# Kernel tuning notes

Hardware: AMD Instinct MI355X
Metric: run time of the kernel (lower is better)

Reference implementation:

```python
import jax, jax.numpy as jnp
import numpy as np

KH, KW = 7, 7            # extraction kernel
EH, EW = 5, 5            # effective (cropped) kernel
PAD = (KH - EH) // 2     # = 1
EPS = 1e-7


def _extract_patches(x):
    # x: [B,H,W,C] -> patches [B,Ho,Wo,KH,KW,C], stride 1, VALID padding
    B, H, Wd, C = x.shape
    Ho, Wo = H - KH + 1, Wd - KW + 1
    rows = []
    for i in range(KH):
        cols = [x[:, i:i + Ho, j:j + Wo, :] for j in range(KW)]
        rows.append(jnp.stack(cols, axis=3))          # [B,Ho,Wo,KW,C]
    return jnp.stack(rows, axis=3)                     # [B,Ho,Wo,KH,KW,C]


def _rotate_bilinear(patches, angles):
    # patches: [N,KH,KW,C]; angles: [N]. Mirrors tf.contrib.image
    # angles_to_projective_transforms + transform(BILINEAR, fill=0).
    # Note: the layer's det(matrix)==0 NEAREST fallback never fires (det==1).
    N = patches.shape[0]
    c, s = jnp.cos(angles), jnp.sin(angles)
    Wm1, Hm1 = jnp.float32(KW - 1), jnp.float32(KH - 1)
    xo = (Wm1 - (c * Wm1 - s * Hm1)) * 0.5
    yo = (Hm1 - (s * Wm1 + c * Hm1)) * 0.5
    scale = jnp.float32(1.0 + EPS)   # transforms /= transforms[:,8:9]+1e-7
    a0, a1, a2 = c / scale, -s / scale, xo / scale
    a3, a4, a5 = s / scale, c / scale, yo / scale
    yg, xg = jnp.meshgrid(jnp.arange(KH, dtype=jnp.float32),
                          jnp.arange(KW, dtype=jnp.float32), indexing='ij')
    x_in = a0[:, None, None] * xg + a1[:, None, None] * yg + a2[:, None, None]
    y_in = a3[:, None, None] * xg + a4[:, None, None] * yg + a5[:, None, None]
    x0f = jnp.floor(x_in); y0f = jnp.floor(y_in)
    wx1 = x_in - x0f; wx0 = 1.0 - wx1
    wy1 = y_in - y0f; wy0 = 1.0 - wy1
    x0 = x0f.astype(jnp.int32); x1 = x0 + 1
    y0 = y0f.astype(jnp.int32); y1 = y0 + 1
    nidx = jnp.arange(N)[:, None, None]

    def corner(yi, xi, w):
        valid = ((xi >= 0) & (xi < KW) & (yi >= 0) & (yi < KH)).astype(patches.dtype)
        v = patches[nidx, jnp.clip(yi, 0, KH - 1), jnp.clip(xi, 0, KW - 1)]
        return (w * valid)[..., None] * v

    return (corner(y0, x0, wy0 * wx0) + corner(y0, x1, wy0 * wx1) +
            corner(y1, x0, wy1 * wx0) + corner(y1, x1, wy1 * wx1))


def reference(x, W, b):
    B, H, Wd, C = x.shape
    patches = _extract_patches(x)                      # [B,Ho,Wo,KH,KW,C]
    _, Ho, Wo = patches.shape[:3]
    intensity = jnp.sum(patches, axis=-1)              # [B,Ho,Wo,KH,KW]
    row_idx = jnp.repeat(jnp.arange(KH, dtype=jnp.float32), KW)   # rowMulti
    col_idx = jnp.tile(jnp.arange(KW, dtype=jnp.float32), KH)     # colMulti
    flat = intensity.reshape(-1, KH * KW)              # [N, KH*KW]
    denom = jnp.sum(flat, -1) + EPS
    cr = jnp.sum(flat * row_idx, -1) / denom - (KH - 1) / 2.0
    cc = jnp.sum(flat * col_idx, -1) / denom - (KW - 1) / 2.0
    angle = jnp.arctan2(cr, cc + EPS)                  # [N]
    patches_n = patches.reshape(-1, KH, KW, C)         # [N,KH,KW,C]
    rot = _rotate_bilinear(patches_n, angle)
    rot = rot[:, PAD:PAD + EH, PAD:PAD + EW, :]        # crop to effective
    rot = rot.reshape(B, Ho, Wo, EH * EW * C)
    w_flat = W.reshape(W.shape[0], -1)                 # [F, EH*EW*C]
    out = jnp.einsum('bhwk,fk->bhwf', rot, w_flat) + b
    return out


def setup_inputs() -> dict:
    key = jax.random.key(0)
    kx, kw, _ = jax.random.split(key, 3)
    x = jax.random.normal(kx, (8, 64, 64, 32), dtype=jnp.float32)
    W = jax.random.normal(kw, (64, EH, EW, 32), dtype=jnp.float32) * 0.05
    b = jnp.zeros((64,), dtype=jnp.float32)
    return {"x": x, "W": W, "b": b}
```

## Files before the change

### kernel.cpp

```cpp
#include <hip/hip_runtime.h>
#include <hip/hip_bf16.h>

#define EPSF 1e-7f
#define B_ 8
#define H_ 64
#define W_ 64
#define C_ 32
#define HO 58
#define WO 58
#define NF 64
#define KDIM 800

#define XTS 36
#define RPS 520

typedef __bf16 v8bf __attribute__((ext_vector_type(8)));
typedef float  v4f  __attribute__((ext_vector_type(4)));

__global__ void k_wpack(const float* __restrict__ W, __bf16* __restrict__ Wp) {
    int t = blockIdx.x*256 + threadIdx.x;
    int j = t & 7; int lane = (t >> 3) & 63; int rest = t >> 9;
    int kb = rest % 25; int nt = rest / 25;
    int f = nt*16 + (lane & 15);
    int k = kb*32 + (lane >> 4)*8 + j;
    Wp[t] = (__bf16)W[f*KDIM + k];
}

__global__ __launch_bounds__(256)
void k_main(const float* __restrict__ x, const v8bf* __restrict__ Wp,
            const float* __restrict__ bias, float* __restrict__ out) {
    __shared__ float  xt[7][22][XTS];
    __shared__ __bf16 rot[25*RPS];
    __shared__ float  Srow[7][22];
    __shared__ float4 pp[16];

    int tid = threadIdx.x;
    int wv = tid >> 6, lane = tid & 63;
    int wt = blockIdx.x, ho = blockIdx.y, b = blockIdx.z;
    int wo0 = wt*16;
    int npx = WO - wo0; if (npx > 16) npx = 16;
    int ncols = npx + 6;

    v8bf bfrag[25];
    {
        const v8bf* wp = Wp + (size_t)wv*25*64 + lane;
#pragma unroll
        for (int kb = 0; kb < 25; kb++) bfrag[kb] = wp[kb*64];
    }

    const float* xb = x + (size_t)((b*H_ + ho)*W_ + wo0)*C_;
    int total4 = 7*ncols*8;
    for (int e = tid; e < total4; e += 256) {
        int r = e/(ncols*8); int rem = e - r*(ncols*8);
        int c = rem >> 3;    int q = rem & 7;
        *(float4*)&xt[r][c][q*4] = *(const float4*)&xb[(r*W_ + c)*C_ + q*4];
    }
    __syncthreads();

    if (tid < 7*ncols) {
        int r = tid / ncols, c = tid - r*ncols;
        float s = 0.f;
#pragma unroll
        for (int q = 0; q < 8; q++) {
            float4 v = *(const float4*)&xt[r][c][q*4];
            s += v.x + v.y + v.z + v.w;
        }
        Srow[r][c] = s;
    }
    __syncthreads();

    if (tid < npx) {
        float den = 0.f, crn = 0.f, ccn = 0.f;
#pragma unroll
        for (int i = 0; i < 7; i++)
#pragma unroll
            for (int j = 0; j < 7; j++) {
                float v = Srow[i][tid + j];
                den += v; crn += v*(float)i; ccn += v*(float)j;
            }
        float dt = den + EPSF;
        float cr = crn/dt - 3.0f;
        float cc = ccn/dt - 3.0f;
        float ang = atan2f(cr, cc + EPSF);
        float c = cosf(ang), s = sinf(ang);
        const float scale = 1.0f + EPSF;
        float xo = (6.0f - (c*6.0f - s*6.0f))*0.5f;
        float yo = (6.0f - (s*6.0f + c*6.0f))*0.5f;
        pp[tid] = make_float4(c/scale, s/scale, xo/scale, yo/scale);
    }
    __syncthreads();

    int tot = npx*25;
    for (int e = tid; e < tot; e += 256) {
        int px = e/25; int pos = e - px*25;
        int py = pos/5; int yy = py + 1; int xx = pos - py*5 + 1;
        float4 p = pp[px];
        float xin = p.x*(float)xx - p.y*(float)yy + p.z;
        float yin = p.y*(float)xx + p.x*(float)yy + p.w;
        float x0f = floorf(xin), y0f = floorf(yin);
        float wx1 = xin - x0f, wx0 = 1.0f - wx1;
        float wy1 = yin - y0f, wy0 = 1.0f - wy1;
        int ix0 = (int)x0f, iy0 = (int)y0f;
        int ix1 = ix0 + 1,  iy1 = iy0 + 1;

        const float* bp[4]; float wgt[4];
        auto mkcorner = [&](int yi, int xi, float w, int idx) {
            bool valid = (xi >= 0) & (xi < 7) & (yi >= 0) & (yi < 7);
            int cy = yi < 0 ? 0 : (yi > 6 ? 6 : yi);
            int cx = xi < 0 ? 0 : (xi > 6 ? 6 : xi);
            bp[idx]  = &xt[cy][px + cx][0];
            wgt[idx] = valid ? w : 0.0f;
        };
        mkcorner(iy0, ix0, wy0*wx0, 0);
        mkcorner(iy0, ix1, wy0*wx1, 1);
        mkcorner(iy1, ix0, wy1*wx0, 2);
        mkcorner(iy1, ix1, wy1*wx1, 3);

        float acc[32];
#pragma unroll
        for (int ch = 0; ch < 32; ch++) acc[ch] = 0.f;
#pragma unroll
        for (int cn = 0; cn < 4; cn++) {
            const float* src = bp[cn]; float wq = wgt[cn];
#pragma unroll
            for (int q = 0; q < 8; q++) {
                float4 v = *(const float4*)(src + q*4);
                acc[q*4+0] += wq*v.x; acc[q*4+1] += wq*v.y;
                acc[q*4+2] += wq*v.z; acc[q*4+3] += wq*v.w;
            }
        }
        __bf16* dst = &rot[pos*RPS + px*32];
#pragma unroll
        for (int q8 = 0; q8 < 4; q8++) {
            v8bf o;
#pragma unroll
            for (int j = 0; j < 8; j++) o[j] = (__bf16)acc[q8*8 + j];
            *(v8bf*)&dst[q8*8] = o;
        }
    }
    __syncthreads();

    int m = lane & 15, q = lane >> 4;
    v4f acc4 = {0.f, 0.f, 0.f, 0.f};
#pragma unroll
    for (int kb = 0; kb < 25; kb++) {
        v8bf a = *(const v8bf*)&rot[kb*RPS + m*32 + q*8];
        acc4 = __builtin_amdgcn_mfma_f32_16x16x32_bf16(a, bfrag[kb], acc4, 0, 0, 0);
    }
    int f = wv*16 + m;
    float bv = bias[f];
    int pixbase = (b*HO + ho)*WO + wo0;
#pragma unroll
    for (int r = 0; r < 4; r++) {
        int px = q*4 + r;
        if (px < npx) out[(size_t)(pixbase + px)*NF + f] = acc4[r] + bv;
    }
}

extern "C" void kernel_launch(void* const* d_in, const int* in_sizes, int n_in,
                              void* d_out, int out_size, void* d_ws, size_t ws_size,
                              hipStream_t stream) {
    const float* x    = (const float*)d_in[0];
    const float* W    = (const float*)d_in[1];
    const float* bias = (const float*)d_in[2];
    float* out = (float*)d_out;
    __bf16* Wp = (__bf16*)d_ws;

    k_wpack<<<dim3(200), 256, 0, stream>>>(W, Wp);
    k_main<<<dim3(4, HO, B_), 256, 0, stream>>>(x, (const v8bf*)Wp, bias, out);
}
```

Measured before the change: 90.94 us.

## Restructure rotated-patch LDS layout, replace atan2 with rsqrt, defer weight loads

Changes the LDS staging buffer for rotated patches from position-major to pixel-major rows padded to 808 elements, and remaps the rotation work so consecutive threads handle consecutive pixels at the same position. Replaces atan2f/cosf/sinf with a direct normalization via rsqrtf to get the cosine and sine of the angle. Moves the 25 weight-fragment global loads to after the rotation stage, which reduces register pressure during that phase. The aim is fewer transcendental instructions, fewer LDS bank conflicts, and better occupancy. The new angle path can differ slightly in rounding from the atan2 path in degenerate cases.

```diff
diff --git a/kernel.cpp b/kernel.cpp
--- a/kernel.cpp
+++ b/kernel.cpp
@@ -12,7 +12,7 @@
 #define KDIM 800
 
 #define XTS 36
-#define RPS 520
+#define RS  808
 
 typedef __bf16 v8bf __attribute__((ext_vector_type(8)));
 typedef float  v4f  __attribute__((ext_vector_type(4)));
@@ -30,30 +30,24 @@
 void k_main(const float* __restrict__ x, const v8bf* __restrict__ Wp,
             const float* __restrict__ bias, float* __restrict__ out) {
     __shared__ float  xt[7][22][XTS];
-    __shared__ __bf16 rot[25*RPS];
+    __shared__ __bf16 rot[16][RS];
     __shared__ float  Srow[7][22];
     __shared__ float4 pp[16];
 
     int tid = threadIdx.x;
     int wv = tid >> 6, lane = tid & 63;
+    int m = lane & 15, q = lane >> 4;
     int wt = blockIdx.x, ho = blockIdx.y, b = blockIdx.z;
     int wo0 = wt*16;
     int npx = WO - wo0; if (npx > 16) npx = 16;
     int ncols = npx + 6;
 
-    v8bf bfrag[25];
-    {
-        const v8bf* wp = Wp + (size_t)wv*25*64 + lane;
-#pragma unroll
-        for (int kb = 0; kb < 25; kb++) bfrag[kb] = wp[kb*64];
-    }
-
     const float* xb = x + (size_t)((b*H_ + ho)*W_ + wo0)*C_;
     int total4 = 7*ncols*8;
     for (int e = tid; e < total4; e += 256) {
         int r = e/(ncols*8); int rem = e - r*(ncols*8);
-        int c = rem >> 3;    int q = rem & 7;
-        *(float4*)&xt[r][c][q*4] = *(const float4*)&xb[(r*W_ + c)*C_ + q*4];
+        int c = rem >> 3;    int qq = rem & 7;
+        *(float4*)&xt[r][c][qq*4] = *(const float4*)&xb[(r*W_ + c)*C_ + qq*4];
     }
     __syncthreads();
 
@@ -61,8 +55,8 @@
         int r = tid / ncols, c = tid - r*ncols;
         float s = 0.f;
 #pragma unroll
-        for (int q = 0; q < 8; q++) {
-            float4 v = *(const float4*)&xt[r][c][q*4];
+        for (int qq = 0; qq < 8; qq++) {
+            float4 v = *(const float4*)&xt[r][c][qq*4];
             s += v.x + v.y + v.z + v.w;
         }
         Srow[r][c] = s;
@@ -80,9 +74,11 @@
             }
         float dt = den + EPSF;
         float cr = crn/dt - 3.0f;
-        float cc = ccn/dt - 3.0f;
-        float ang = atan2f(cr, cc + EPSF);
-        float c = cosf(ang), s = sinf(ang);
+        float cx = ccn/dt - 3.0f + EPSF;
+        float r2 = cr*cr + cx*cx;
+        float inv = r2 > 0.f ? rsqrtf(r2) : 0.f;
+        float c = r2 > 0.f ? cx*inv : 1.0f;
+        float s = cr*inv;
         const float scale = 1.0f + EPSF;
         float xo = (6.0f - (c*6.0f - s*6.0f))*0.5f;
         float yo = (6.0f - (s*6.0f + c*6.0f))*0.5f;
@@ -90,61 +86,68 @@
     }
     __syncthreads();
 
-    int tot = npx*25;
-    for (int e = tid; e < tot; e += 256) {
-        int px = e/25; int pos = e - px*25;
-        int py = pos/5; int yy = py + 1; int xx = pos - py*5 + 1;
-        float4 p = pp[px];
-        float xin = p.x*(float)xx - p.y*(float)yy + p.z;
-        float yin = p.y*(float)xx + p.x*(float)yy + p.w;
-        float x0f = floorf(xin), y0f = floorf(yin);
-        float wx1 = xin - x0f, wx0 = 1.0f - wx1;
-        float wy1 = yin - y0f, wy0 = 1.0f - wy1;
-        int ix0 = (int)x0f, iy0 = (int)y0f;
-        int ix1 = ix0 + 1,  iy1 = iy0 + 1;
+    for (int e = tid; e < 400; e += 256) {
+        int px = e & 15; int pos = e >> 4;
+        if (px < npx) {
+            int py = pos/5; int yy = py + 1; int xx = pos - py*5 + 1;
+            float4 p = pp[px];
+            float xin = p.x*(float)xx - p.y*(float)yy + p.z;
+            float yin = p.y*(float)xx + p.x*(float)yy + p.w;
+            float x0f = floorf(xin), y0f = floorf(yin);
+            float wx1 = xin - x0f, wx0 = 1.0f - wx1;
+            float wy1 = yin - y0f, wy0 = 1.0f - wy1;
+            int ix0 = (int)x0f, iy0 = (int)y0f;
+            int ix1 = ix0 + 1,  iy1 = iy0 + 1;
 
-        const float* bp[4]; float wgt[4];
-        auto mkcorner = [&](int yi, int xi, float w, int idx) {
-            bool valid = (xi >= 0) & (xi < 7) & (yi >= 0) & (yi < 7);
-            int cy = yi < 0 ? 0 : (yi > 6 ? 6 : yi);
-            int cx = xi < 0 ? 0 : (xi > 6 ? 6 : xi);
-            bp[idx]  = &xt[cy][px + cx][0];
-            wgt[idx] = valid ? w : 0.0f;
-        };
-        mkcorner(iy0, ix0, wy0*wx0, 0);
-        mkcorner(iy0, ix1, wy0*wx1, 1);
-        mkcorner(iy1, ix0, wy1*wx0, 2);
-        mkcorner(iy1, ix1, wy1*wx1, 3);
+            const float* bp[4]; float wgt[4];
+            auto mkcorner = [&](int yi, int xi, float w, int idx) {
+                bool valid = (xi >= 0) & (xi < 7) & (yi >= 0) & (yi < 7);
+                int cy = yi < 0 ? 0 : (yi > 6 ? 6 : yi);
+                int cx2 = xi < 0 ? 0 : (xi > 6 ? 6 : xi);
+                bp[idx]  = &xt[cy][px + cx2][0];
+                wgt[idx] = valid ? w : 0.0f;
+            };
+            mkcorner(iy0, ix0, wy0*wx0, 0);
+            mkcorner(iy0, ix1, wy0*wx1, 1);
+            mkcorner(iy1, ix0, wy1*wx0, 2);
+            mkcorner(iy1, ix1, wy1*wx1, 3);
 
-        float acc[32];
+            float acc[32];
 #pragma unroll
-        for (int ch = 0; ch < 32; ch++) acc[ch] = 0.f;
+            for (int ch = 0; ch < 32; ch++) acc[ch] = 0.f;
 #pragma unroll
-        for (int cn = 0; cn < 4; cn++) {
-            const float* src = bp[cn]; float wq = wgt[cn];
+            for (int cn = 0; cn < 4; cn++) {
+                const float* src = bp[cn]; float wq = wgt[cn];
 #pragma unroll
-            for (int q = 0; q < 8; q++) {
-                float4 v = *(const float4*)(src + q*4);
-                acc[q*4+0] += wq*v.x; acc[q*4+1] += wq*v.y;
-                acc[q*4+2] += wq*v.z; acc[q*4+3] += wq*v.w;
+                for (int qq = 0; qq < 8; qq++) {
+                    float4 v = *(const float4*)(src + qq*4);
+                    acc[qq*4+0] += wq*v.x; acc[qq*4+1] += wq*v.y;
+                    acc[qq*4+2] += wq*v.z; acc[qq*4+3] += wq*v.w;
+                }
+            }
+            __bf16* dst = &rot[px][pos*32];
+#pragma unroll
+            for (int q8 = 0; q8 < 4; q8++) {
+                v8bf o;
+#pragma unroll
+                for (int j = 0; j < 8; j++) o[j] = (__bf16)acc[q8*8 + j];
+                *(v8bf*)&dst[q8*8] = o;
             }
         }
-        __bf16* dst = &rot[pos*RPS + px*32];
+    }
+
+    v8bf bfrag[25];
+    {
+        const v8bf* wp = Wp + (size_t)wv*25*64 + lane;
 #pragma unroll
-        for (int q8 = 0; q8 < 4; q8++) {
-            v8bf o;
-#pragma unroll
-            for (int j = 0; j < 8; j++) o[j] = (__bf16)acc[q8*8 + j];
-            *(v8bf*)&dst[q8*8] = o;
-        }
+        for (int kb = 0; kb < 25; kb++) bfrag[kb] = wp[kb*64];
     }
     __syncthreads();
 
-    int m = lane & 15, q = lane >> 4;
     v4f acc4 = {0.f, 0.f, 0.f, 0.f};
 #pragma unroll
     for (int kb = 0; kb < 25; kb++) {
-        v8bf a = *(const v8bf*)&rot[kb*RPS + m*32 + q*8];
+        v8bf a = *(const v8bf*)&rot[m][kb*32 + q*8];
         acc4 = __builtin_amdgcn_mfma_f32_16x16x32_bf16(a, bfrag[kb], acc4, 0, 0, 0);
     }
     int f = wv*16 + m;
```

Result: faster. 83.46 us (-8.2%).
